# Performance work log

Measured on AMD Instinct MI355X. Metric: run time of the kernel, lower is better.

Reference implementation:

```python
import jax, jax.numpy as jnp
import numpy as np

HIDDEN = 4096
N_HEADS = 32
N_KV_HEADS = 8
HEAD_DIM = HIDDEN // N_HEADS  # 128
INTER = 11008
EPS = 1e-6
ROPE_THETA = 10000.0
B, S = 2, 2048


def setup_inputs() -> dict:
    key = jax.random.key(0)
    ks = jax.random.split(key, 8)
    sc = 0.02
    return {
        "hidden_states": jax.random.normal(ks[0], (B, S, HIDDEN), dtype=jnp.float32),
        "positions": jnp.arange(S, dtype=jnp.int32),
        "w_qkv": jax.random.normal(ks[1], (HIDDEN, (N_HEADS + 2 * N_KV_HEADS) * HEAD_DIM), dtype=jnp.float32) * sc,
        "w_o": jax.random.normal(ks[2], (N_HEADS * HEAD_DIM, HIDDEN), dtype=jnp.float32) * sc,
        "w_gate_up": jax.random.normal(ks[3], (HIDDEN, 2 * INTER), dtype=jnp.float32) * sc,
        "w_down": jax.random.normal(ks[4], (INTER, HIDDEN), dtype=jnp.float32) * sc,
        "ln1_w": jnp.ones((HIDDEN,), dtype=jnp.float32),
        "ln2_w": jnp.ones((HIDDEN,), dtype=jnp.float32),
    }


def _rms_norm(x, w):
    var = jnp.mean(jnp.square(x), axis=-1, keepdims=True)
    return x * jax.lax.rsqrt(var + EPS) * w


def _rope(x, positions):
    # x: [B, S, H, D]; NeoX-style rotary over full head_dim
    d = x.shape[-1]
    inv_freq = 1.0 / (ROPE_THETA ** (jnp.arange(0, d, 2, dtype=jnp.float32) / d))
    freqs = positions.astype(jnp.float32)[:, None] * inv_freq[None, :]  # [S, D/2]
    cos = jnp.cos(freqs)[None, :, None, :]
    sin = jnp.sin(freqs)[None, :, None, :]
    x1, x2 = jnp.split(x, 2, axis=-1)
    return jnp.concatenate([x1 * cos - x2 * sin, x2 * cos + x1 * sin], axis=-1)


def _decoder_layer(hidden_states, positions, w_qkv, w_o, w_gate_up, w_down, ln1_w, ln2_w):
    b, s, _ = hidden_states.shape
    scale = HEAD_DIM ** -0.5

    # --- attention block ---
    residual = hidden_states
    x = _rms_norm(hidden_states, ln1_w)
    qkv = x @ w_qkv
    q, k, v = jnp.split(qkv, [N_HEADS * HEAD_DIM, (N_HEADS + N_KV_HEADS) * HEAD_DIM], axis=-1)
    q = q.reshape(b, s, N_HEADS, HEAD_DIM)
    k = k.reshape(b, s, N_KV_HEADS, HEAD_DIM)
    v = v.reshape(b, s, N_KV_HEADS, HEAD_DIM)
    q = _rope(q, positions)
    k = _rope(k, positions)
    # GQA: expand kv heads
    g = N_HEADS // N_KV_HEADS
    k = jnp.repeat(k, g, axis=2)  # [B, S, H, D]
    v = jnp.repeat(v, g, axis=2)
    scores = jnp.einsum("bqhd,bkhd->bhqk", q, k) * scale
    causal = jnp.tril(jnp.ones((s, s), dtype=bool))
    scores = jnp.where(causal[None, None], scores, jnp.finfo(scores.dtype).min)
    probs = jax.nn.softmax(scores, axis=-1)
    attn = jnp.einsum("bhqk,bkhd->bqhd", probs, v).reshape(b, s, N_HEADS * HEAD_DIM)
    hidden_states = residual + attn @ w_o

    # --- MLP block (SwiGLU) ---
    residual = hidden_states
    x = _rms_norm(hidden_states, ln2_w)
    gate_up = x @ w_gate_up
    gate, up = jnp.split(gate_up, 2, axis=-1)
    hidden_states = residual + (jax.nn.silu(gate) * up) @ w_down
    return hidden_states


def reference(hidden_states, positions, w_qkv, w_o, w_gate_up, w_down, ln1_w, ln2_w):
    return _decoder_layer(hidden_states, positions, w_qkv, w_o, w_gate_up, w_down, ln1_w, ln2_w)
```

## Files before the change

kernel.cpp:

```cpp
#include <hip/hip_runtime.h>


typedef __attribute__((ext_vector_type(8))) short bf16x8;
typedef __attribute__((ext_vector_type(4))) float f32x4;

__device__ __forceinline__ ushort f2bf(float f) {
  unsigned u = __float_as_uint(f);
  return (ushort)((u + 0x7fffu + ((u >> 16) & 1u)) >> 16);
}
__device__ __forceinline__ float bf2f(ushort u) {
  union { unsigned u32; float f; } x; x.u32 = ((unsigned)u) << 16; return x.f;
}
__device__ __forceinline__ void gload16(const void* g, void* l) {
  __builtin_amdgcn_global_load_lds((__attribute__((address_space(1))) void*)g,
                                   (__attribute__((address_space(3))) void*)l,
                                   16, 0, 0);
}

#define BARRIER() asm volatile("s_barrier" ::: "memory")
#define WAIT_LGKM0() asm volatile("s_waitcnt lgkmcnt(0)" ::: "memory")
#define WAIT_VM4() asm volatile("s_waitcnt vmcnt(4)" ::: "memory")
#define WAIT_VM0() asm volatile("s_waitcnt vmcnt(0)" ::: "memory")

__global__ __launch_bounds__(256) void rmsnorm_kernel(
    const float* __restrict__ x, const float* __restrict__ g,
    ushort* __restrict__ out) {
  const int row = blockIdx.x, t = threadIdx.x;
  const float4* xp = (const float4*)(x + (size_t)row * 4096);
  float4 v[4]; float ss = 0.f;
#pragma unroll
  for (int i = 0; i < 4; ++i) {
    v[i] = xp[t + i * 256];
    ss += v[i].x * v[i].x + v[i].y * v[i].y + v[i].z * v[i].z + v[i].w * v[i].w;
  }
#pragma unroll
  for (int m = 32; m; m >>= 1) ss += __shfl_xor(ss, m);
  __shared__ float red[4];
  if ((t & 63) == 0) red[t >> 6] = ss;
  __syncthreads();
  float inv = rsqrtf((red[0] + red[1] + red[2] + red[3]) * (1.f / 4096.f) + 1e-6f);
  const float4* gp = (const float4*)g;
  ushort* op = out + (size_t)row * 4096;
#pragma unroll
  for (int i = 0; i < 4; ++i) {
    float4 gv = gp[t + i * 256];
    ushort4 o;
    o.x = f2bf(v[i].x * inv * gv.x); o.y = f2bf(v[i].y * inv * gv.y);
    o.z = f2bf(v[i].z * inv * gv.z); o.w = f2bf(v[i].w * inv * gv.w);
    *(ushort4*)(op + (size_t)(t + i * 256) * 4) = o;
  }
}

__global__ __launch_bounds__(256) void transpose_cast_kernel(
    const float* __restrict__ in, ushort* __restrict__ out,
    int ld_in, int col_off, int R) {
  __shared__ ushort tile[64][68];
  const int t = threadIdx.x;
  const int r0 = blockIdx.x * 64, c0 = blockIdx.y * 64;
  const int rl = t >> 2, cl = (t & 3) * 16;
  const float* ip = in + (size_t)(r0 + rl) * ld_in + col_off + c0 + cl;
#pragma unroll
  for (int i = 0; i < 4; ++i) {
    float4 f = ((const float4*)ip)[i];
    tile[rl][cl + i * 4 + 0] = f2bf(f.x);
    tile[rl][cl + i * 4 + 1] = f2bf(f.y);
    tile[rl][cl + i * 4 + 2] = f2bf(f.z);
    tile[rl][cl + i * 4 + 3] = f2bf(f.w);
  }
  __syncthreads();
  union { ushort us[8]; uint4 v; } pk0, pk1;
#pragma unroll
  for (int j = 0; j < 8; ++j) pk0.us[j] = tile[cl + j][rl];
#pragma unroll
  for (int j = 0; j < 8; ++j) pk1.us[j] = tile[cl + 8 + j][rl];
  uint4* op = (uint4*)(out + (size_t)(c0 + rl) * R + r0 + cl);
  op[0] = pk0.v; op[1] = pk1.v;
}

template <typename OutT, bool RES>
__global__ __launch_bounds__(512, 2) void gemm256_kernel(
    const ushort* __restrict__ A, const ushort* __restrict__ Bt,
    OutT* __restrict__ C, const float* __restrict__ res,
    int M, int N, int K) {
  extern __shared__ ushort lds[];
  ushort* Al = lds;
  ushort* Bl = lds + 32768;
  const int t = threadIdx.x, l = t & 63, w = t >> 6;
  const int wr = w >> 2, wc = w & 3;
  const int lr = l & 15, lg = l >> 4;
  const int rhi = lr >> 3, rlo = lr & 7;
  const int srow = l >> 3, sg = (l & 7) ^ srow;

  const int nbx = N >> 8;
  const int nwg = nbx * (M >> 8);
  const int cpx = nwg >> 3;
  const int bid = (int)blockIdx.x;
  const int swz = (bid & 7) * cpx + (bid >> 3);
  const int n0 = (swz % nbx) << 8, m0 = (swz / nbx) << 8;

  const int lof0 = rhi * 512 + rlo * 64 + ((0 + lg) ^ rlo) * 8;
  const int lof1 = rhi * 512 + rlo * 64 + ((4 + lg) ^ rlo) * 8;

  const f32x4 fz = {0.f, 0.f, 0.f, 0.f};
  f32x4 acc[8][4];
#pragma unroll
  for (int i = 0; i < 8; ++i)
#pragma unroll
    for (int j = 0; j < 4; ++j) acc[i][j] = fz;
  bf16x8 a[8][2];
  bf16x8 bq[2][2];

  const ushort* Asrc = A + (size_t)(m0 + w * 8 + srow) * K + sg * 8;
  const ushort* Bsrc = Bt + (size_t)(n0 + w * 8 + srow) * K + sg * 8;
  const size_t rK64 = (size_t)64 * K, rK128 = (size_t)128 * K;
  ushort* Adst = Al + w * 512;
  ushort* Bdst = Bl + w * 512;

#define STAGE_A(buf, half, tile) do {                                   \
    const ushort* s_ = Asrc + (size_t)(half) * rK128 + ((tile) << 6);   \
    ushort* d_ = Adst + (buf) * 16384 + (half) * 8192;                  \
    gload16(s_, d_);                                                    \
    gload16(s_ + rK64, d_ + 4096);                                      \
  } while (0)
#define STAGE_B(buf, half, tile) do {                                   \
    const ushort* s_ = Bsrc + (size_t)(half) * rK128 + ((tile) << 6);   \
    ushort* d_ = Bdst + (buf) * 16384 + (half) * 8192;                  \
    gload16(s_, d_);                                                    \
    gload16(s_ + rK64, d_ + 4096);                                      \
  } while (0)
#define LDA4(AH, QM) do {                                                   \
    _Pragma("unroll") for (int mi_ = 0; mi_ < 4; ++mi_) {                   \
      a[(QM) * 4 + mi_][0] =                                                \
          *(const bf16x8*)((AH) + ((QM) * 4 + mi_) * 1024 + lof0);          \
      a[(QM) * 4 + mi_][1] =                                                \
          *(const bf16x8*)((AH) + ((QM) * 4 + mi_) * 1024 + lof1);          \
    } } while (0)
#define LDB2(BH, NQ) do {                                                   \
    _Pragma("unroll") for (int nj_ = 0; nj_ < 2; ++nj_) {                   \
      bq[nj_][0] = *(const bf16x8*)((BH) + ((NQ) * 2 + nj_) * 1024 + lof0); \
      bq[nj_][1] = *(const bf16x8*)((BH) + ((NQ) * 2 + nj_) * 1024 + lof1); \
    } } while (0)
#define MFMA16(QM, QN)                                                      \
    __builtin_amdgcn_s_setprio(1);                                          \
    _Pragma("unroll") for (int mi_ = 0; mi_ < 4; ++mi_)                     \
    _Pragma("unroll") for (int nj_ = 0; nj_ < 2; ++nj_) {                   \
      acc[(QM) * 4 + mi_][(QN) * 2 + nj_] =                                 \
          __builtin_amdgcn_mfma_f32_16x16x32_bf16(                          \
              a[(QM) * 4 + mi_][0], bq[nj_][0],                             \
              acc[(QM) * 4 + mi_][(QN) * 2 + nj_], 0, 0, 0);                \
      acc[(QM) * 4 + mi_][(QN) * 2 + nj_] =                                 \
          __builtin_amdgcn_mfma_f32_16x16x32_bf16(                          \
              a[(QM) * 4 + mi_][1], bq[nj_][1],                             \
              acc[(QM) * 4 + mi_][(QN) * 2 + nj_], 0, 0, 0);                \
    }                                                                       \
    __builtin_amdgcn_s_setprio(0);

  const ushort* A0h = Al + wr * 8192;
  const ushort* A1h = A0h + 16384;
  const ushort* B0h = Bl + (wc >> 1) * 8192 + (wc & 1) * 4096;
  const ushort* B1h = B0h + 16384;

  const int ntiles = K >> 6, nIter = K >> 7;
  STAGE_A(0, 0, 0); STAGE_A(0, 1, 0); STAGE_B(0, 0, 0); STAGE_B(0, 1, 0);
  STAGE_A(1, 0, 1); STAGE_A(1, 1, 1);
  WAIT_VM4(); BARRIER();

  for (int it = 0; it < nIter; ++it) {
    const int u = it * 2;
    LDA4(A0h, 0); LDB2(B0h, 0);
    STAGE_B(1, 0, u + 1);
    BARRIER(); WAIT_LGKM0(); MFMA16(0, 0); BARRIER();
    LDA4(A0h, 1);
    STAGE_B(1, 1, u + 1);
    BARRIER(); WAIT_LGKM0(); MFMA16(1, 0); BARRIER();
    LDB2(B0h, 1);
    if (u + 2 < ntiles) STAGE_A(0, 0, u + 2);
    BARRIER(); WAIT_LGKM0(); MFMA16(0, 1); BARRIER();
    if (u + 2 < ntiles) STAGE_A(0, 1, u + 2);
    BARRIER(); MFMA16(1, 1);
    if (u + 2 < ntiles) { WAIT_VM4(); } else { WAIT_VM0(); }
    BARRIER();
    LDA4(A1h, 0); LDB2(B1h, 0);
    if (u + 2 < ntiles) STAGE_B(0, 0, u + 2);
    BARRIER(); WAIT_LGKM0(); MFMA16(0, 0); BARRIER();
    LDA4(A1h, 1);
    if (u + 2 < ntiles) STAGE_B(0, 1, u + 2);
    BARRIER(); WAIT_LGKM0(); MFMA16(1, 0); BARRIER();
    LDB2(B1h, 1);
    if (u + 3 < ntiles) STAGE_A(1, 0, u + 3);
    BARRIER(); WAIT_LGKM0(); MFMA16(0, 1); BARRIER();
    if (u + 3 < ntiles) STAGE_A(1, 1, u + 3);
    BARRIER(); MFMA16(1, 1);
    WAIT_VM4(); BARRIER();
  }

#pragma unroll
  for (int mi = 0; mi < 8; ++mi)
#pragma unroll
    for (int ni = 0; ni < 4; ++ni)
#pragma unroll
      for (int r = 0; r < 4; ++r) {
        int row = m0 + wr * 128 + mi * 16 + lg * 4 + r;
        int col = n0 + wc * 64 + ni * 16 + lr;
        size_t idx = (size_t)row * N + col;
        float v = acc[mi][ni][r];
        if (RES) v += res[idx];
        if constexpr (sizeof(OutT) == 2) C[idx] = f2bf(v);
        else                             C[idx] = v;
      }
#undef STAGE_A
#undef STAGE_B
#undef LDA4
#undef LDB2
#undef MFMA16
}

__global__ void rope_table_kernel(const int* __restrict__ pos,
                                  float2* __restrict__ tab) {
  int idx = blockIdx.x * 256 + threadIdx.x;
  int s = idx >> 6, fi = idx & 63;
  float inv = (float)exp(-(double)(2 * fi) / 128.0 * 9.210340371976184);
  float a = (float)pos[s] * inv;
  tab[idx] = make_float2(cosf(a), sinf(a));
}

__global__ __launch_bounds__(256) void rope_scatter_kernel(
    const ushort* __restrict__ qkv, const float2* __restrict__ tab,
    ushort* __restrict__ Qr, ushort* __restrict__ Kr, ushort* __restrict__ Vt) {
  __shared__ ushort vt[64][132];
  const int t = threadIdx.x, tt = blockIdx.x, h = blockIdx.y;
  const int row = t >> 2, c = (t & 3) * 16;
  const int tok = tt * 64 + row;
  const int b = tok >> 11, s = tok & 2047;
  const ushort* ip = qkv + (size_t)tok * 6144 + h * 128;
  union U { uint4 v; ushort us[8]; };
  U a0, a1, b0, b1;
  a0.v = *(const uint4*)(ip + c);      a1.v = *(const uint4*)(ip + c + 8);
  b0.v = *(const uint4*)(ip + c + 64); b1.v = *(const uint4*)(ip + c + 72);
  if (h < 40) {
    U o0, o1, o2, o3;
#pragma unroll
    for (int j = 0; j < 8; ++j) {
      float2 cs = tab[s * 64 + c + j];
      float x1 = bf2f(a0.us[j]), x2 = bf2f(b0.us[j]);
      o0.us[j] = f2bf(x1 * cs.x - x2 * cs.y);
      o2.us[j] = f2bf(x2 * cs.x + x1 * cs.y);
    }
#pragma unroll
    for (int j = 0; j < 8; ++j) {
      float2 cs = tab[s * 64 + c + 8 + j];
      float x1 = bf2f(a1.us[j]), x2 = bf2f(b1.us[j]);
      o1.us[j] = f2bf(x1 * cs.x - x2 * cs.y);
      o3.us[j] = f2bf(x2 * cs.x + x1 * cs.y);
    }
    ushort* base;
    if (h < 32) base = Qr + ((size_t)((b * 32 + h) * 2048 + s)) * 128;
    else        base = Kr + ((size_t)((b * 8 + (h - 32)) * 2048 + s)) * 128;
    *(uint4*)(base + c)      = o0.v; *(uint4*)(base + c + 8)  = o1.v;
    *(uint4*)(base + c + 64) = o2.v; *(uint4*)(base + c + 72) = o3.v;
  } else {
    const int hv = h - 40;
#pragma unroll
    for (int j = 0; j < 8; ++j) {
      vt[row][c + j]      = a0.us[j]; vt[row][c + 8 + j]  = a1.us[j];
      vt[row][c + 64 + j] = b0.us[j]; vt[row][c + 72 + j] = b1.us[j];
    }
    __syncthreads();
    const int d = t >> 1, s0 = (t & 1) * 32, sb = (tt & 31) * 64;
    U w0, w1, w2, w3;
#pragma unroll
    for (int j = 0; j < 8; ++j) {
      w0.us[j] = vt[s0 + j][d];      w1.us[j] = vt[s0 + 8 + j][d];
      w2.us[j] = vt[s0 + 16 + j][d]; w3.us[j] = vt[s0 + 24 + j][d];
    }
    ushort* vb = Vt + ((size_t)((b * 8 + hv) * 128 + d)) * 2048 + sb + s0;
    *(uint4*)(vb) = w0.v;      *(uint4*)(vb + 8) = w1.v;
    *(uint4*)(vb + 16) = w2.v; *(uint4*)(vb + 24) = w3.v;
  }
}

__global__ __launch_bounds__(256) void attn_kernel(
    const ushort* __restrict__ Q, const ushort* __restrict__ K,
    const ushort* __restrict__ V, ushort* __restrict__ O) {
  __shared__ ushort Kl[64 * 128];
  __shared__ ushort Vl[128 * 64];
  __shared__ ushort Pl[64 * 64];
  const int t = threadIdx.x, l = t & 63, w = t >> 6;
  const int lr = l & 15, lg = l >> 4, lk = lg * 8;
  const int qt = blockIdx.x, h = blockIdx.y, b = blockIdx.z;
  const int hkv = h >> 2;
  const f32x4 fzero = {0.f, 0.f, 0.f, 0.f};

  const ushort* qp =
      Q + ((size_t)((b * 32 + h) * 2048 + qt * 64 + w * 16 + lr)) * 128 + lk;
  bf16x8 qf[4];
#pragma unroll
  for (int ks = 0; ks < 4; ++ks) qf[ks] = *(const bf16x8*)(qp + ks * 32);

  const ushort* kg = K + ((size_t)(b * 8 + hkv)) * 2048 * 128;
  const ushort* vg = V + ((size_t)(b * 8 + hkv)) * 128 * 2048;

  f32x4 accO[8];
#pragma unroll
  for (int i = 0; i < 8; ++i) accO[i] = fzero;
  float m_r[4] = {-1e30f, -1e30f, -1e30f, -1e30f};
  float l_r[4] = {0.f, 0.f, 0.f, 0.f};
  const float scale = 0.08838834764831845f;
  const int qrow = qt * 64 + w * 16 + lg * 4;

  for (int j = 0; j <= qt; ++j) {
    const int s0 = j * 64;
#pragma unroll
    for (int i = 0; i < 4; ++i)
      gload16(kg + (size_t)(s0 + ((i * 256 + t) >> 4)) * 128 + (t & 15) * 8,
              (char*)Kl + i * 4096 + t * 16);
#pragma unroll
    for (int i = 0; i < 4; ++i)
      gload16(vg + (size_t)((i * 256 + t) >> 3) * 2048 + s0 + (t & 7) * 8,
              (char*)Vl + i * 4096 + t * 16);
    __syncthreads();

    f32x4 sc[4];
#pragma unroll
    for (int ni = 0; ni < 4; ++ni) sc[ni] = fzero;
#pragma unroll
    for (int ni = 0; ni < 4; ++ni)
#pragma unroll
      for (int ks = 0; ks < 4; ++ks) {
        bf16x8 kf = *(const bf16x8*)(Kl + (ni * 16 + lr) * 128 + ks * 32 + lk);
        sc[ni] = __builtin_amdgcn_mfma_f32_16x16x32_bf16(qf[ks], kf, sc[ni], 0, 0, 0);
      }
#pragma unroll
    for (int ni = 0; ni < 4; ++ni)
#pragma unroll
      for (int r = 0; r < 4; ++r) {
        float v = sc[ni][r] * scale;
        if (s0 + ni * 16 + lr > qrow + r) v = -1e30f;
        sc[ni][r] = v;
      }
    float mnew[4], fsc[4], lad[4];
#pragma unroll
    for (int r = 0; r < 4; ++r) {
      float mx = fmaxf(fmaxf(sc[0][r], sc[1][r]), fmaxf(sc[2][r], sc[3][r]));
#pragma unroll
      for (int m = 8; m; m >>= 1) mx = fmaxf(mx, __shfl_xor(mx, m));
      mnew[r] = fmaxf(m_r[r], mx);
      fsc[r] = __expf(m_r[r] - mnew[r]);
      lad[r] = 0.f;
    }
#pragma unroll
    for (int ni = 0; ni < 4; ++ni)
#pragma unroll
      for (int r = 0; r < 4; ++r) {
        float p = __expf(sc[ni][r] - mnew[r]);
        sc[ni][r] = p;
        lad[r] += p;
      }
#pragma unroll
    for (int r = 0; r < 4; ++r) {
#pragma unroll
      for (int m = 8; m; m >>= 1) lad[r] += __shfl_xor(lad[r], m);
      l_r[r] = l_r[r] * fsc[r] + lad[r];
      m_r[r] = mnew[r];
    }
#pragma unroll
    for (int i = 0; i < 8; ++i)
#pragma unroll
      for (int r = 0; r < 4; ++r) accO[i][r] *= fsc[r];
#pragma unroll
    for (int ni = 0; ni < 4; ++ni)
#pragma unroll
      for (int r = 0; r < 4; ++r)
        Pl[(w * 16 + lg * 4 + r) * 64 + ni * 16 + lr] = f2bf(sc[ni][r]);
    asm volatile("s_waitcnt lgkmcnt(0)" ::: "memory");
#pragma unroll
    for (int ks = 0; ks < 2; ++ks) {
      bf16x8 pf = *(const bf16x8*)(Pl + (w * 16 + lr) * 64 + ks * 32 + lk);
#pragma unroll
      for (int nf = 0; nf < 8; ++nf) {
        bf16x8 vf = *(const bf16x8*)(Vl + (nf * 16 + lr) * 64 + ks * 32 + lk);
        accO[nf] = __builtin_amdgcn_mfma_f32_16x16x32_bf16(pf, vf, accO[nf], 0, 0, 0);
      }
    }
    __syncthreads();
  }
#pragma unroll
  for (int nf = 0; nf < 8; ++nf)
#pragma unroll
    for (int r = 0; r < 4; ++r) {
      int q = qt * 64 + w * 16 + lg * 4 + r;
      int d = nf * 16 + lr;
      float v = accO[nf][r] / l_r[r];
      O[((size_t)(b * 2048 + q)) * 4096 + h * 128 + d] = f2bf(v);
    }
}

__global__ void swiglu_kernel(ushort* __restrict__ gate,
                              const ushort* __restrict__ up, int n8) {
  union U { uint4 v; ushort us[8]; };
  for (int i = blockIdx.x * blockDim.x + threadIdx.x; i < n8;
       i += gridDim.x * blockDim.x) {
    U gv, uv, ov;
    gv.v = ((const uint4*)gate)[i];
    uv.v = ((const uint4*)up)[i];
#pragma unroll
    for (int j = 0; j < 8; ++j) {
      float x = bf2f(gv.us[j]);
      float y = bf2f(uv.us[j]);
      ov.us[j] = f2bf(x / (1.f + __expf(-x)) * y);
    }
    ((uint4*)gate)[i] = ov.v;
  }
}

#define OFF_W    ((size_t)0)
#define OFF_H1   ((size_t)90177536)
#define OFF_XN   ((size_t)157286400)
#define OFF_QKV  ((size_t)190840832)
#define OFF_TAB  ((size_t)241172480)
#define OFF_QR   ((size_t)242221056)
#define OFF_KR   ((size_t)275775488)
#define OFF_VT   ((size_t)284164096)
#define OFF_ATTN ((size_t)292552704)
#define OFF_GATE OFF_QKV
#define OFF_UP   ((size_t)326107136)
#define WS_NEED  ((size_t)416284672)

extern "C" void kernel_launch(void* const* d_in, const int* in_sizes, int n_in,
                              void* d_out, int out_size, void* d_ws,
                              size_t ws_size, hipStream_t stream) {
  (void)in_sizes; (void)n_in; (void)out_size;
  if (ws_size < WS_NEED) return;
  const float* hs     = (const float*)d_in[0];
  const int*   pos    = (const int*)d_in[1];
  const float* w_qkv  = (const float*)d_in[2];
  const float* w_o    = (const float*)d_in[3];
  const float* w_gu   = (const float*)d_in[4];
  const float* w_down = (const float*)d_in[5];
  const float* ln1    = (const float*)d_in[6];
  const float* ln2    = (const float*)d_in[7];
  float* out = (float*)d_out;
  char* ws = (char*)d_ws;

  ushort* W    = (ushort*)(ws + OFF_W);
  float*  h1   = (float*)(ws + OFF_H1);
  ushort* xn   = (ushort*)(ws + OFF_XN);
  ushort* qkv  = (ushort*)(ws + OFF_QKV);
  float2* tab  = (float2*)(ws + OFF_TAB);
  ushort* Qr   = (ushort*)(ws + OFF_QR);
  ushort* Kr   = (ushort*)(ws + OFF_KR);
  ushort* Vt   = (ushort*)(ws + OFF_VT);
  ushort* attn = (ushort*)(ws + OFF_ATTN);
  ushort* gate = (ushort*)(ws + OFF_GATE);
  ushort* up   = (ushort*)(ws + OFF_UP);

  auto kb = gemm256_kernel<ushort, false>;
  auto kf = gemm256_kernel<float, true>;
  hipFuncSetAttribute((const void*)kb, hipFuncAttributeMaxDynamicSharedMemorySize, 131072);
  hipFuncSetAttribute((const void*)kf, hipFuncAttributeMaxDynamicSharedMemorySize, 131072);

  rmsnorm_kernel<<<4096, 256, 0, stream>>>(hs, ln1, xn);
  transpose_cast_kernel<<<dim3(64, 96), 256, 0, stream>>>(w_qkv, W, 6144, 0, 4096);
  gemm256_kernel<ushort, false><<<384, 512, 131072, stream>>>(
      xn, W, qkv, nullptr, 4096, 6144, 4096);
  rope_table_kernel<<<512, 256, 0, stream>>>(pos, tab);
  rope_scatter_kernel<<<dim3(64, 48), 256, 0, stream>>>(qkv, tab, Qr, Kr, Vt);
  attn_kernel<<<dim3(32, 32, 2), 256, 0, stream>>>(Qr, Kr, Vt, attn);
  transpose_cast_kernel<<<dim3(64, 64), 256, 0, stream>>>(w_o, W, 4096, 0, 4096);
  gemm256_kernel<float, true><<<256, 512, 131072, stream>>>(
      attn, W, h1, hs, 4096, 4096, 4096);

  rmsnorm_kernel<<<4096, 256, 0, stream>>>(h1, ln2, xn);
  transpose_cast_kernel<<<dim3(64, 172), 256, 0, stream>>>(w_gu, W, 22016, 0, 4096);
  gemm256_kernel<ushort, false><<<688, 512, 131072, stream>>>(
      xn, W, gate, nullptr, 4096, 11008, 4096);
  transpose_cast_kernel<<<dim3(64, 172), 256, 0, stream>>>(w_gu, W, 22016, 11008, 4096);
  gemm256_kernel<ushort, false><<<688, 512, 131072, stream>>>(
      xn, W, up, nullptr, 4096, 11008, 4096);
  swiglu_kernel<<<2048, 256, 0, stream>>>(gate, up, (4096 * 11008) / 8);
  transpose_cast_kernel<<<dim3(172, 64), 256, 0, stream>>>(w_down, W, 4096, 0, 11008);
  gemm256_kernel<float, true><<<256, 512, 131072, stream>>>(
      gate, W, out, h1, 4096, 4096, 11008);
}
```

Before: 2.105 ms.

## Double-buffer K/V tiles in attention with swizzled LDS and mask only diagonal

The attention kernel now keeps two K/V buffers in dynamic LDS and prefetches the next tile with async global-to-LDS loads while the current tile is computed, waiting with partial vmcnt. K, V and P LDS layouts are XOR-swizzled to cut bank conflicts, the causal mask is applied only on the diagonal tile, and setprio is raised around the MFMA sections. LDS per block grows to about 72KB, which may limit blocks per CU.

New measurement: 1.911 ms. 9.2% less time.

```diff
diff --git a/kernel.cpp b/kernel.cpp
--- a/kernel.cpp
+++ b/kernel.cpp
@@ -19,6 +19,7 @@
 
 #define BARRIER() asm volatile("s_barrier" ::: "memory")
 #define WAIT_LGKM0() asm volatile("s_waitcnt lgkmcnt(0)" ::: "memory")
+#define WAIT_VM8() asm volatile("s_waitcnt vmcnt(8)" ::: "memory")
 #define WAIT_VM4() asm volatile("s_waitcnt vmcnt(4)" ::: "memory")
 #define WAIT_VM0() asm volatile("s_waitcnt vmcnt(0)" ::: "memory")
 
@@ -282,23 +283,43 @@
 __global__ __launch_bounds__(256) void attn_kernel(
     const ushort* __restrict__ Q, const ushort* __restrict__ K,
     const ushort* __restrict__ V, ushort* __restrict__ O) {
-  __shared__ ushort Kl[64 * 128];
-  __shared__ ushort Vl[128 * 64];
-  __shared__ ushort Pl[64 * 64];
+  extern __shared__ ushort sm[];
+  ushort* Kl = sm;
+  ushort* Vl = sm + 16384;
+  ushort* Pl = sm + 32768;
   const int t = threadIdx.x, l = t & 63, w = t >> 6;
-  const int lr = l & 15, lg = l >> 4, lk = lg * 8;
+  const int lr = l & 15, lg = l >> 4;
   const int qt = blockIdx.x, h = blockIdx.y, b = blockIdx.z;
   const int hkv = h >> 2;
   const f32x4 fzero = {0.f, 0.f, 0.f, 0.f};
 
+  const int rm = lr & 7;
+  int ksw[4], vsw[2];
+#pragma unroll
+  for (int ks = 0; ks < 4; ++ks) ksw[ks] = ((ks * 4 + lg) ^ rm) * 8;
+  vsw[0] = (lg ^ rm) * 8;
+  vsw[1] = ((4 + lg) ^ rm) * 8;
+  const int kcol = ((t & 15) ^ ((t >> 4) & 7)) * 8;
+  const int vcol = ((t & 7) ^ ((t >> 3) & 7)) * 8;
+
   const ushort* qp =
-      Q + ((size_t)((b * 32 + h) * 2048 + qt * 64 + w * 16 + lr)) * 128 + lk;
+      Q + ((size_t)((b * 32 + h) * 2048 + qt * 64 + w * 16 + lr)) * 128 + lg * 8;
   bf16x8 qf[4];
 #pragma unroll
   for (int ks = 0; ks < 4; ++ks) qf[ks] = *(const bf16x8*)(qp + ks * 32);
+  WAIT_VM0();
 
   const ushort* kg = K + ((size_t)(b * 8 + hkv)) * 2048 * 128;
   const ushort* vg = V + ((size_t)(b * 8 + hkv)) * 128 * 2048;
+
+#define STAGE_KV(buf, s0_) do {                                              \
+    _Pragma("unroll") for (int i_ = 0; i_ < 4; ++i_)                         \
+      gload16(kg + (size_t)((s0_) + i_ * 16 + (t >> 4)) * 128 + kcol,        \
+              (char*)Kl + (buf) * 16384 + i_ * 4096 + t * 16);               \
+    _Pragma("unroll") for (int i_ = 0; i_ < 4; ++i_)                         \
+      gload16(vg + (size_t)(i_ * 32 + (t >> 3)) * 2048 + (s0_) + vcol,       \
+              (char*)Vl + (buf) * 16384 + i_ * 4096 + t * 16);               \
+  } while (0)
 
   f32x4 accO[8];
 #pragma unroll
@@ -308,36 +329,41 @@
   const float scale = 0.08838834764831845f;
   const int qrow = qt * 64 + w * 16 + lg * 4;
 
+  STAGE_KV(0, 0);
   for (int j = 0; j <= qt; ++j) {
-    const int s0 = j * 64;
-#pragma unroll
-    for (int i = 0; i < 4; ++i)
-      gload16(kg + (size_t)(s0 + ((i * 256 + t) >> 4)) * 128 + (t & 15) * 8,
-              (char*)Kl + i * 4096 + t * 16);
-#pragma unroll
-    for (int i = 0; i < 4; ++i)
-      gload16(vg + (size_t)((i * 256 + t) >> 3) * 2048 + s0 + (t & 7) * 8,
-              (char*)Vl + i * 4096 + t * 16);
-    __syncthreads();
+    if (j < qt) { STAGE_KV((j + 1) & 1, (j + 1) * 64); WAIT_VM8(); }
+    else        { WAIT_VM0(); }
+    BARRIER();
+    const ushort* Kb = Kl + (j & 1) * 8192;
+    const ushort* Vb = Vl + (j & 1) * 8192;
 
     f32x4 sc[4];
 #pragma unroll
     for (int ni = 0; ni < 4; ++ni) sc[ni] = fzero;
+    __builtin_amdgcn_s_setprio(1);
 #pragma unroll
     for (int ni = 0; ni < 4; ++ni)
 #pragma unroll
       for (int ks = 0; ks < 4; ++ks) {
-        bf16x8 kf = *(const bf16x8*)(Kl + (ni * 16 + lr) * 128 + ks * 32 + lk);
+        bf16x8 kf = *(const bf16x8*)(Kb + (ni * 16 + lr) * 128 + ksw[ks]);
         sc[ni] = __builtin_amdgcn_mfma_f32_16x16x32_bf16(qf[ks], kf, sc[ni], 0, 0, 0);
       }
-#pragma unroll
-    for (int ni = 0; ni < 4; ++ni)
-#pragma unroll
-      for (int r = 0; r < 4; ++r) {
-        float v = sc[ni][r] * scale;
-        if (s0 + ni * 16 + lr > qrow + r) v = -1e30f;
-        sc[ni][r] = v;
-      }
+    __builtin_amdgcn_s_setprio(0);
+    if (j == qt) {
+#pragma unroll
+      for (int ni = 0; ni < 4; ++ni)
+#pragma unroll
+        for (int r = 0; r < 4; ++r) {
+          float v = sc[ni][r] * scale;
+          if (j * 64 + ni * 16 + lr > qrow + r) v = -1e30f;
+          sc[ni][r] = v;
+        }
+    } else {
+#pragma unroll
+      for (int ni = 0; ni < 4; ++ni)
+#pragma unroll
+        for (int r = 0; r < 4; ++r) sc[ni][r] *= scale;
+    }
     float mnew[4], fsc[4], lad[4];
 #pragma unroll
     for (int r = 0; r < 4; ++r) {
@@ -370,20 +396,26 @@
 #pragma unroll
     for (int ni = 0; ni < 4; ++ni)
 #pragma unroll
-      for (int r = 0; r < 4; ++r)
-        Pl[(w * 16 + lg * 4 + r) * 64 + ni * 16 + lr] = f2bf(sc[ni][r]);
-    asm volatile("s_waitcnt lgkmcnt(0)" ::: "memory");
+      for (int r = 0; r < 4; ++r) {
+        int prow = w * 16 + lg * 4 + r;
+        int slot = (ni * 2 + (lr >> 3)) ^ (prow & 7);
+        Pl[prow * 64 + slot * 8 + rm] = f2bf(sc[ni][r]);
+      }
+    WAIT_LGKM0();
+    __builtin_amdgcn_s_setprio(1);
 #pragma unroll
     for (int ks = 0; ks < 2; ++ks) {
-      bf16x8 pf = *(const bf16x8*)(Pl + (w * 16 + lr) * 64 + ks * 32 + lk);
+      bf16x8 pf = *(const bf16x8*)(Pl + (w * 16 + lr) * 64 + vsw[ks]);
 #pragma unroll
       for (int nf = 0; nf < 8; ++nf) {
-        bf16x8 vf = *(const bf16x8*)(Vl + (nf * 16 + lr) * 64 + ks * 32 + lk);
+        bf16x8 vf = *(const bf16x8*)(Vb + (nf * 16 + lr) * 64 + vsw[ks]);
         accO[nf] = __builtin_amdgcn_mfma_f32_16x16x32_bf16(pf, vf, accO[nf], 0, 0, 0);
       }
     }
-    __syncthreads();
-  }
+    __builtin_amdgcn_s_setprio(0);
+    BARRIER();
+  }
+#undef STAGE_KV
 #pragma unroll
   for (int nf = 0; nf < 8; ++nf)
 #pragma unroll
@@ -458,6 +490,7 @@
   auto kf = gemm256_kernel<float, true>;
   hipFuncSetAttribute((const void*)kb, hipFuncAttributeMaxDynamicSharedMemorySize, 131072);
   hipFuncSetAttribute((const void*)kf, hipFuncAttributeMaxDynamicSharedMemorySize, 131072);
+  hipFuncSetAttribute((const void*)attn_kernel, hipFuncAttributeMaxDynamicSharedMemorySize, 73728);
 
   rmsnorm_kernel<<<4096, 256, 0, stream>>>(hs, ln1, xn);
   transpose_cast_kernel<<<dim3(64, 96), 256, 0, stream>>>(w_qkv, W, 6144, 0, 4096);
@@ -465,7 +498,7 @@
       xn, W, qkv, nullptr, 4096, 6144, 4096);
   rope_table_kernel<<<512, 256, 0, stream>>>(pos, tab);
   rope_scatter_kernel<<<dim3(64, 48), 256, 0, stream>>>(qkv, tab, Qr, Kr, Vt);
-  attn_kernel<<<dim3(32, 32, 2), 256, 0, stream>>>(Qr, Kr, Vt, attn);
+  attn_kernel<<<dim3(32, 32, 2), 256, 73728, stream>>>(Qr, Kr, Vt, attn);
   transpose_cast_kernel<<<dim3(64, 64), 256, 0, stream>>>(w_o, W, 4096, 0, 4096);
   gemm256_kernel<float, true><<<256, 512, 131072, stream>>>(
       attn, W, h1, hs, 4096, 4096, 4096);
```
